# Kernel optimization log

Hardware: AMD Instinct MI355X
Metric: run time of the kernel (lower is better)

## Reference

```python
import jax, jax.numpy as jnp
import numpy as np

KERNEL_SIZE = 128
NEG_INF = -1e30


def setup_inputs() -> dict:
    key = jax.random.key(0)
    ks = jax.random.split(key, 5)
    B, S, D, H = 4, 4096, 512, 512
    x = jax.random.normal(ks[0], (B, S, D), dtype=jnp.float32)
    # torch nn.Linear weights: [out_features, in_features], y = x @ W.T + b
    Wq_w = jax.random.normal(ks[1], (H, D), dtype=jnp.float32) * (1.0 / np.sqrt(D))
    Wq_b = jax.random.normal(ks[2], (H,), dtype=jnp.float32) * 0.01
    Wk_w = jax.random.normal(ks[3], (H, D), dtype=jnp.float32) * (1.0 / np.sqrt(D))
    Wk_b = jax.random.normal(ks[4], (H,), dtype=jnp.float32) * 0.01
    return {"x": x, "Wq_w": Wq_w, "Wq_b": Wq_b, "Wk_w": Wk_w, "Wk_b": Wk_b}


def reference(x, Wq_w, Wq_b, Wk_w, Wk_b):
    # q, k: [B, S, H]
    q = jnp.einsum('bsd,hd->bsh', x, Wq_w) + Wq_b
    k = jnp.einsum('bsd,hd->bsh', x, Wk_w) + Wk_b
    # dense scores [B, S, S]
    scores = jnp.einsum('bih,bjh->bij', q, k)
    # band mask: True where i-kernel_size+1 <= j <= i+kernel_size-1
    idx = jnp.arange(x.shape[1])
    band = jnp.abs(idx[:, None] - idx[None, :]) < KERNEL_SIZE  # [S, S]
    scores = jnp.where(band[None, :, :], scores, NEG_INF)
    attn = jax.nn.softmax(scores, axis=2)
    # attend over raw x (no V projection in original module)
    return jnp.einsum('bij,bjd->bid', attn, x)
```

## Files before the change

kernel.cpp:

```cpp
#include <hip/hip_runtime.h>
#include <hip/hip_bf16.h>

#define S_LEN 4096
#define NEG_INF_F (-1e30f)

typedef __attribute__((ext_vector_type(4))) float f32x4;
typedef __attribute__((ext_vector_type(8))) short s16x8;
typedef unsigned short u16;

static __device__ __forceinline__ u16 f2bf(float f) {
    unsigned u = __builtin_bit_cast(unsigned, f);
    unsigned r = u + 0x7FFFu + ((u >> 16) & 1u);
    return (u16)(r >> 16);
}
static __device__ __forceinline__ float bf2f(u16 h) {
    unsigned u = ((unsigned)h) << 16;
    return __builtin_bit_cast(float, u);
}
static __device__ __forceinline__ void split4(const float4 v, ushort4& hi, ushort4& lo) {
    hi.x = f2bf(v.x); lo.x = f2bf(v.x - bf2f(hi.x));
    hi.y = f2bf(v.y); lo.y = f2bf(v.y - bf2f(hi.y));
    hi.z = f2bf(v.z); lo.z = f2bf(v.z - bf2f(hi.z));
    hi.w = f2bf(v.w); lo.w = f2bf(v.w - bf2f(hi.w));
}
static __device__ __forceinline__ void gl_lds16(const void* g, void* l) {
    __builtin_amdgcn_global_load_lds(
        (const __attribute__((address_space(1))) void*)g,
        (__attribute__((address_space(3))) void*)l, 16, 0, 0);
}
static __device__ __forceinline__ int swz64(int row, int col_u16) {
    return row * 64 + (col_u16 ^ ((row & 7) << 3));
}
static __device__ __forceinline__ int swz32(int row, int col_u16) {
    return row * 32 + (col_u16 ^ (((row >> 1) & 3) << 3));
}
static __device__ __forceinline__ int swz320(int row, int col_u16) {
    return row * 320 + (col_u16 ^ ((row & 7) << 3));
}
static __device__ __forceinline__ int xcd_swz512(int bid) {
    return (bid & 7) * 64 + (bid >> 3);
}
static __device__ __forceinline__ int xcd_swz256(int bid) {
    return (bid & 7) * 32 + (bid >> 3);
}

__global__ __launch_bounds__(256) void prep_kernel(
    const float* __restrict__ x, const float* __restrict__ Wk,
    const float* __restrict__ Wq, const float* __restrict__ bq,
    u16* __restrict__ xh, u16* __restrict__ xl, u16* __restrict__ xT,
    u16* __restrict__ Mth, u16* __restrict__ Mtl, float* __restrict__ uvec) {
    __shared__ __align__(16) u16 sm[9216];
    const int bid = blockIdx.x;
    const int tid = threadIdx.x;

    if (bid < 256) {
        const int bm = bid & 15, bn = bid >> 4;
        const int m0 = bm * 32, n0 = bn * 32;
        u16* Ath = sm;
        u16* Atl = sm + 2304;
        u16* Bth = sm + 4608;
        u16* Btl = sm + 6912;
        const int lane = tid & 63, w = tid >> 6;
        const int rg = w >> 1, cg = w & 1;
        const int frow = lane & 15, fk = (lane >> 4) * 8;
        f32x4 acc = {};

        for (int h0 = 0; h0 < 512; h0 += 64) {
            #pragma unroll
            for (int i = 0; i < 2; ++i) {
                int idx = i * 256 + tid;
                int h = idx >> 3, c4 = (idx & 7) * 4;
                float4 a = *(const float4*)(Wk + (size_t)(h0 + h) * 512 + m0 + c4);
                ushort4 ahi, alo; split4(a, ahi, alo);
                Ath[(c4 + 0) * 72 + h] = ahi.x; Atl[(c4 + 0) * 72 + h] = alo.x;
                Ath[(c4 + 1) * 72 + h] = ahi.y; Atl[(c4 + 1) * 72 + h] = alo.y;
                Ath[(c4 + 2) * 72 + h] = ahi.z; Atl[(c4 + 2) * 72 + h] = alo.z;
                Ath[(c4 + 3) * 72 + h] = ahi.w; Atl[(c4 + 3) * 72 + h] = alo.w;
                float4 b = *(const float4*)(Wq + (size_t)(h0 + h) * 512 + n0 + c4);
                ushort4 bhi, blo; split4(b, bhi, blo);
                Bth[(c4 + 0) * 72 + h] = bhi.x; Btl[(c4 + 0) * 72 + h] = blo.x;
                Bth[(c4 + 1) * 72 + h] = bhi.y; Btl[(c4 + 1) * 72 + h] = blo.y;
                Bth[(c4 + 2) * 72 + h] = bhi.z; Btl[(c4 + 2) * 72 + h] = blo.z;
                Bth[(c4 + 3) * 72 + h] = bhi.w; Btl[(c4 + 3) * 72 + h] = blo.w;
            }
            __syncthreads();
            #pragma unroll
            for (int kk = 0; kk < 2; ++kk) {
                s16x8 aH = *(const s16x8*)&Ath[(rg * 16 + frow) * 72 + kk * 32 + fk];
                s16x8 aL = *(const s16x8*)&Atl[(rg * 16 + frow) * 72 + kk * 32 + fk];
                s16x8 bH = *(const s16x8*)&Bth[(cg * 16 + frow) * 72 + kk * 32 + fk];
                s16x8 bL = *(const s16x8*)&Btl[(cg * 16 + frow) * 72 + kk * 32 + fk];
                acc = __builtin_amdgcn_mfma_f32_16x16x32_bf16(aH, bH, acc, 0, 0, 0);
                acc = __builtin_amdgcn_mfma_f32_16x16x32_bf16(aH, bL, acc, 0, 0, 0);
                acc = __builtin_amdgcn_mfma_f32_16x16x32_bf16(aL, bH, acc, 0, 0, 0);
            }
            __syncthreads();
        }
        int d1 = n0 + cg * 16 + frow;
        #pragma unroll
        for (int e = 0; e < 4; ++e) {
            int d2 = m0 + rg * 16 + (lane >> 4) * 4 + e;
            float v = acc[e];
            u16 hi = f2bf(v);
            Mth[(size_t)d2 * 512 + d1] = hi;
            Mtl[(size_t)d2 * 512 + d1] = f2bf(v - bf2f(hi));
        }
    } else if (bid < 264) {
        const int ub = bid - 256;
        float* red = (float*)sm;
        const int c = tid & 63, hg = tid >> 6;
        const int d2 = ub * 64 + c;
        float acc = 0.f;
        for (int h = hg; h < 512; h += 4) acc += Wk[(size_t)h * 512 + d2] * bq[h];
        red[hg * 64 + c] = acc;
        __syncthreads();
        if (hg == 0)
            uvec[d2] = red[0 * 64 + c] + red[1 * 64 + c] + red[2 * 64 + c] + red[3 * 64 + c];
    } else {
        const int sb = bid - 264;
        const int dt = sb & 7, st = (sb >> 3) & 63, b = sb >> 9;
        const int s0 = st * 64, d0 = dt * 64;
        u16 (*T)[74] = (u16(*)[74])sm;
        #pragma unroll
        for (int i = 0; i < 2; ++i) {
            int idx = i * 256 + tid;
            int r = idx >> 3, c8 = (idx & 7) * 8;
            const float* src = x + (size_t)(b * S_LEN + s0 + r) * 512 + d0 + c8;
            float4 v0 = *(const float4*)(src);
            float4 v1 = *(const float4*)(src + 4);
            ushort4 h0, l0, h1, l1;
            split4(v0, h0, l0);
            split4(v1, h1, l1);
            s16x8 hv, lv;
            hv[0] = (short)h0.x; hv[1] = (short)h0.y; hv[2] = (short)h0.z; hv[3] = (short)h0.w;
            hv[4] = (short)h1.x; hv[5] = (short)h1.y; hv[6] = (short)h1.z; hv[7] = (short)h1.w;
            lv[0] = (short)l0.x; lv[1] = (short)l0.y; lv[2] = (short)l0.z; lv[3] = (short)l0.w;
            lv[4] = (short)l1.x; lv[5] = (short)l1.y; lv[6] = (short)l1.z; lv[7] = (short)l1.w;
            *(s16x8*)(xh + (size_t)(b * S_LEN + s0 + r) * 512 + d0 + c8) = hv;
            *(s16x8*)(xl + (size_t)(b * S_LEN + s0 + r) * 512 + d0 + c8) = lv;
            unsigned* tp = (unsigned*)&T[r][c8];
            tp[0] = (unsigned)(u16)hv[0] | ((unsigned)(u16)hv[1] << 16);
            tp[1] = (unsigned)(u16)hv[2] | ((unsigned)(u16)hv[3] << 16);
            tp[2] = (unsigned)(u16)hv[4] | ((unsigned)(u16)hv[5] << 16);
            tp[3] = (unsigned)(u16)hv[6] | ((unsigned)(u16)hv[7] << 16);
        }
        __syncthreads();
        {
            const int drp = tid >> 3, sc = tid & 7;
            s16x8 v0, v1;
            #pragma unroll
            for (int t = 0; t < 8; ++t) {
                unsigned wv = *(const unsigned*)&T[sc * 8 + t][drp * 2];
                v0[t] = (short)(wv & 0xFFFFu);
                v1[t] = (short)(wv >> 16);
            }
            size_t base = (size_t)(b * 512 + d0 + drp * 2) * S_LEN + s0 + sc * 8;
            *(s16x8*)&xT[base] = v0;
            *(s16x8*)&xT[base + S_LEN] = v1;
        }
    }
}

__global__ __launch_bounds__(512) void z_kernel(
    const u16* __restrict__ xh, const u16* __restrict__ xl,
    const u16* __restrict__ Mth, const u16* __restrict__ Mtl,
    const float* __restrict__ u, u16* __restrict__ zh, u16* __restrict__ zl) {
    const int w_ = xcd_swz512((int)blockIdx.x);
    const int bm = w_ >> 2, bn = w_ & 3;
    const int m0 = bm * 128, n0 = bn * 128;
    __shared__ __align__(16) u16 Ah[128 * 64], Al[128 * 64];
    __shared__ __align__(16) u16 Bh[128 * 64], Bl[128 * 64];
    const int tid = threadIdx.x, lane = tid & 63, w = tid >> 6;
    const int rg = w >> 2, cg = w & 3;
    const int frow = lane & 15, fk = (lane >> 4) * 8;
    f32x4 acc[4][2] = {};

    for (int k0 = 0; k0 < 512; k0 += 64) {
        #pragma unroll
        for (int i = 0; i < 2; ++i) {
            int idx = i * 512 + tid;
            int r = idx >> 3, c = idx & 7;
            int sc = (c ^ (r & 7)) * 8;
            gl_lds16(xh + (size_t)(m0 + r) * 512 + k0 + sc, &Ah[idx * 8]);
            gl_lds16(xl + (size_t)(m0 + r) * 512 + k0 + sc, &Al[idx * 8]);
            gl_lds16(Mth + (size_t)(n0 + r) * 512 + k0 + sc, &Bh[idx * 8]);
            gl_lds16(Mtl + (size_t)(n0 + r) * 512 + k0 + sc, &Bl[idx * 8]);
        }
        __syncthreads();
        #pragma unroll
        for (int kk = 0; kk < 2; ++kk) {
            s16x8 aH[4], aL[4], bH[2], bL[2];
            #pragma unroll
            for (int mi = 0; mi < 4; ++mi) {
                int row = rg * 64 + mi * 16 + frow;
                aH[mi] = *(const s16x8*)&Ah[swz64(row, kk * 32 + fk)];
                aL[mi] = *(const s16x8*)&Al[swz64(row, kk * 32 + fk)];
            }
            #pragma unroll
            for (int ni = 0; ni < 2; ++ni) {
                int row = cg * 32 + ni * 16 + frow;
                bH[ni] = *(const s16x8*)&Bh[swz64(row, kk * 32 + fk)];
                bL[ni] = *(const s16x8*)&Bl[swz64(row, kk * 32 + fk)];
            }
            #pragma unroll
            for (int mi = 0; mi < 4; ++mi)
                #pragma unroll
                for (int ni = 0; ni < 2; ++ni) {
                    acc[mi][ni] = __builtin_amdgcn_mfma_f32_16x16x32_bf16(aH[mi], bH[ni], acc[mi][ni], 0, 0, 0);
                    acc[mi][ni] = __builtin_amdgcn_mfma_f32_16x16x32_bf16(aH[mi], bL[ni], acc[mi][ni], 0, 0, 0);
                    acc[mi][ni] = __builtin_amdgcn_mfma_f32_16x16x32_bf16(aL[mi], bH[ni], acc[mi][ni], 0, 0, 0);
                }
        }
        __syncthreads();
    }
    #pragma unroll
    for (int ni = 0; ni < 2; ++ni) {
        int col = n0 + cg * 32 + ni * 16 + frow;
        float uv = u[col];
        #pragma unroll
        for (int mi = 0; mi < 4; ++mi) {
            int rbase = m0 + rg * 64 + mi * 16 + (lane >> 4) * 4;
            #pragma unroll
            for (int e = 0; e < 4; ++e) {
                float v = acc[mi][ni][e] + uv;
                u16 hi = f2bf(v);
                zh[(size_t)(rbase + e) * 512 + col] = hi;
                zl[(size_t)(rbase + e) * 512 + col] = f2bf(v - bf2f(hi));
            }
        }
    }
}

__global__ __launch_bounds__(1024, 4) void attn_kernel(
    const u16* __restrict__ zh, const u16* __restrict__ zl,
    const u16* __restrict__ xh, const u16* __restrict__ xl,
    const u16* __restrict__ xT, float* __restrict__ out) {
    const int w_ = xcd_swz256((int)blockIdx.x);
    const int b = w_ >> 6, it = w_ & 63;
    const int i0 = it * 64, j0 = i0 - 128;
    const int mrow0 = b * S_LEN + i0;

    __shared__ __align__(16) u16 smem[61440];

    const int tid = threadIdx.x, lane = tid & 63, w = tid >> 6;
    const int g = w >> 2, q = w & 3;
    const int frow = lane & 15, fk = (lane >> 4) * 8;
    const int tstart = g + q * 4;
    const int nt = (q == 3) ? 5 : 4;
    const size_t qoff = (size_t)(mrow0 + g * 16 + frow) * 512;
    const int rq = (lane >> 4) * 4;

    f32x4 acc[5] = {};
    s16x8 kr[5];

    auto kload = [&](int s) {
        const int k0 = s * 64;
        #pragma unroll
        for (int i = 0; i < 5; ++i) {
            int f = i * 1024 + tid;
            int idx = (f < 2560) ? f : f - 2560;
            int r = idx >> 3, c = idx & 7;
            int j = min(max(j0 + r, 0), S_LEN - 1);
            const u16* src = (f < 2560) ? xh : xl;
            kr[i] = *(const s16x8*)(src + (size_t)(b * S_LEN + j) * 512 + k0 + c * 8);
        }
    };
    auto kwrite = [&]() {
        #pragma unroll
        for (int i = 0; i < 5; ++i) {
            int f = i * 1024 + tid;
            int idx = (f < 2560) ? f : f - 2560;
            int r = idx >> 3, c = idx & 7;
            int off = ((f < 2560) ? 0 : 20480) + swz64(r, c * 8);
            *(s16x8*)&smem[off] = kr[i];
        }
    };
    auto qkstep = [&](int t) {
        const int k0 = t * 64;
        s16x8 zH0 = *(const s16x8*)(zh + qoff + k0 + fk);
        s16x8 zH1 = *(const s16x8*)(zh + qoff + k0 + 32 + fk);
        s16x8 zL0 = *(const s16x8*)(zl + qoff + k0 + fk);
        s16x8 zL1 = *(const s16x8*)(zl + qoff + k0 + 32 + fk);
        __builtin_amdgcn_s_setprio(1);
        #pragma unroll
        for (int kk = 0; kk < 2; ++kk) {
            s16x8 aH = kk ? zH1 : zH0;
            s16x8 aL = kk ? zL1 : zL0;
            #pragma unroll
            for (int tt = 0; tt < 5; ++tt) {
                if (tt < nt) {
                    int krow = (tstart + tt) * 16 + frow;
                    s16x8 bH = *(const s16x8*)&smem[swz64(krow, kk * 32 + fk)];
                    s16x8 bL = *(const s16x8*)&smem[20480 + swz64(krow, kk * 32 + fk)];
                    acc[tt] = __builtin_amdgcn_mfma_f32_16x16x32_bf16(aH, bH, acc[tt], 0, 0, 0);
                    acc[tt] = __builtin_amdgcn_mfma_f32_16x16x32_bf16(aH, bL, acc[tt], 0, 0, 0);
                    acc[tt] = __builtin_amdgcn_mfma_f32_16x16x32_bf16(aL, bH, acc[tt], 0, 0, 0);
                }
            }
        }
        __builtin_amdgcn_s_setprio(0);
    };

    kload(0);
    for (int t = 0; t < 8; ++t) {
        __syncthreads();
        kwrite();
        __syncthreads();
        if (t < 7) kload(t + 1);
        qkstep(t);
    }

    s16x8 vreg[3];
    auto vload = [&](int ds) {
        const int d0 = ds * 64;
        #pragma unroll
        for (int i = 0; i < 3; ++i) {
            int f = i * 1024 + tid;
            if (f < 2560) {
                int dr = f / 40, c8 = f - dr * 40;
                int jb = j0 + c8 * 8;
                jb = min(max(jb, 0), S_LEN - 8);
                vreg[i] = *(const s16x8*)&xT[(size_t)(b * 512 + d0 + dr) * S_LEN + jb];
            }
        }
    };
    auto vwrite = [&](int vbase) {
        #pragma unroll
        for (int i = 0; i < 3; ++i) {
            int f = i * 1024 + tid;
            if (f < 2560) {
                int dr = f / 40, c8 = f - dr * 40;
                *(s16x8*)&smem[vbase + swz320(dr, c8 * 8)] = vreg[i];
            }
        }
    };
    vload(0);

    float* sred_max = (float*)&smem[40960];
    float* sred_sum = sred_max + 256;
    #pragma unroll
    for (int e = 0; e < 4; ++e) {
        int r = g * 16 + rq + e;
        float m = NEG_INF_F;
        #pragma unroll
        for (int tt = 0; tt < 5; ++tt) {
            if (tt < nt) {
                int jj = (tstart + tt) * 16 + frow;
                int dj = jj - r, j = j0 + jj;
                if (dj >= 1 && dj <= 255 && j >= 0 && j < S_LEN) m = fmaxf(m, acc[tt][e]);
            }
        }
        #pragma unroll
        for (int d = 1; d < 16; d <<= 1) m = fmaxf(m, __shfl_xor(m, d));
        if (frow == 0) sred_max[r * 4 + q] = m;
    }
    __syncthreads();
    float sh[4];
    #pragma unroll
    for (int e = 0; e < 4; ++e) {
        int r = g * 16 + rq + e;
        float mx = fmaxf(fmaxf(sred_max[r * 4], sred_max[r * 4 + 1]),
                         fmaxf(sred_max[r * 4 + 2], sred_max[r * 4 + 3]));
        float s = 0.f;
        #pragma unroll
        for (int tt = 0; tt < 5; ++tt) {
            float pv = 0.f;
            if (tt < nt) {
                int jj = (tstart + tt) * 16 + frow;
                int dj = jj - r, j = j0 + jj;
                bool valid = (dj >= 1 && dj <= 255 && j >= 0 && j < S_LEN);
                pv = valid ? __expf(acc[tt][e] - mx) : 0.f;
            }
            acc[tt][e] = pv;
            s += pv;
        }
        #pragma unroll
        for (int d = 1; d < 16; d <<= 1) s += __shfl_xor(s, d);
        sh[e] = s;
    }
    if (frow == 0) {
        #pragma unroll
        for (int e = 0; e < 4; ++e) sred_sum[(g * 16 + rq + e) * 4 + q] = sh[e];
    }
    __syncthreads();
    float invv[4];
    #pragma unroll
    for (int e = 0; e < 4; ++e) {
        int r = g * 16 + rq + e;
        invv[e] = 1.f / (sred_sum[r * 4] + sred_sum[r * 4 + 1] +
                         sred_sum[r * 4 + 2] + sred_sum[r * 4 + 3]);
    }
    __syncthreads();
    #pragma unroll
    for (int tt = 0; tt < 5; ++tt) {
        if (tt < nt) {
            int t = tstart + tt;
            #pragma unroll
            for (int e = 0; e < 4; ++e) {
                int r = g * 16 + rq + e;
                smem[swz320(r, t * 16 + frow)] = f2bf(acc[tt][e] * invv[e]);
            }
        }
    }
    if (q == 0) {
        for (int t = 0; t < g; ++t)
            #pragma unroll
            for (int e = 0; e < 4; ++e)
                smem[swz320(g * 16 + rq + e, t * 16 + frow)] = 0;
    }
    if (q == 3) {
        for (int t = g + 17; t < 20; ++t)
            #pragma unroll
            for (int e = 0; e < 4; ++e)
                smem[swz320(g * 16 + rq + e, t * 16 + frow)] = 0;
    }
    __syncthreads();

    vwrite(20480);
    vload(1);
    __syncthreads();

    s16x8 afrag[10];
    #pragma unroll
    for (int jt = 0; jt < 10; ++jt)
        afrag[jt] = *(const s16x8*)&smem[swz320(g * 16 + frow, jt * 32 + fk)];

    for (int ds = 0; ds < 8; ++ds) {
        const int cur = 20480 + (ds & 1) * 20480;
        const int nxt = 20480 + ((ds + 1) & 1) * 20480;
        if (ds < 7) {
            vwrite(nxt);
            if (ds < 6) vload(ds + 2);
        }
        f32x4 po = {};
        __builtin_amdgcn_s_setprio(1);
        #pragma unroll
        for (int jt = 0; jt < 10; ++jt) {
            s16x8 bv = *(const s16x8*)&smem[cur + swz320(q * 16 + frow, jt * 32 + fk)];
            po = __builtin_amdgcn_mfma_f32_16x16x32_bf16(afrag[jt], bv, po, 0, 0, 0);
        }
        __builtin_amdgcn_s_setprio(0);
        #pragma unroll
        for (int e = 0; e < 4; ++e) {
            int r = mrow0 + g * 16 + rq + e;
            out[(size_t)r * 512 + ds * 64 + q * 16 + frow] = po[e];
        }
        __syncthreads();
    }
}

extern "C" void kernel_launch(void* const* d_in, const int* in_sizes, int n_in,
                              void* d_out, int out_size, void* d_ws, size_t ws_size,
                              hipStream_t stream) {
    const float* x  = (const float*)d_in[0];
    const float* Wq = (const float*)d_in[1];
    const float* bq = (const float*)d_in[2];
    const float* Wk = (const float*)d_in[3];
    const float* bk = (const float*)d_in[4];
    (void)bk;
    float* out = (float*)d_out;

    u16* xh  = (u16*)d_ws;
    u16* xl  = xh + (size_t)8388608;
    u16* zh  = xl + (size_t)8388608;
    u16* zl  = zh + (size_t)8388608;
    u16* Mth = zl + (size_t)8388608;
    u16* Mtl = Mth + (size_t)262144;
    u16* xT  = Mtl + (size_t)262144;
    float* uv = (float*)(xT + (size_t)8388608);

    hipLaunchKernelGGL(prep_kernel, dim3(2312), dim3(256), 0, stream,
                       x, Wk, Wq, bq, xh, xl, xT, Mth, Mtl, uv);
    hipLaunchKernelGGL(z_kernel, dim3(512), dim3(512), 0, stream,
                       xh, xl, Mth, Mtl, uv, zh, zl);
    hipLaunchKernelGGL(attn_kernel, dim3(256), dim3(1024), 0, stream,
                       zh, zl, xh, xl, xT, out);
}
```

Baseline: 115.9 us.

## Move x transpose out of prep kernel into the z GEMM launch

The transposed bf16 copy of x (xT) is no longer built in the prep kernel. Extra blocks appended to the z GEMM kernel now build it, reading the bf16 xh already written by prep and transposing it through LDS, two tiles per 512-thread block. This shortens the prep kernel and lets the transpose fill the GEMM's grid, at the cost of re-reading xh from memory and a larger, mixed-role launch. The z GEMM blocks now use 64KB of shared memory held in one array.

```diff
diff --git a/kernel.cpp b/kernel.cpp
--- a/kernel.cpp
+++ b/kernel.cpp
@@ -31,9 +31,6 @@
 static __device__ __forceinline__ int swz64(int row, int col_u16) {
     return row * 64 + (col_u16 ^ ((row & 7) << 3));
 }
-static __device__ __forceinline__ int swz32(int row, int col_u16) {
-    return row * 32 + (col_u16 ^ (((row >> 1) & 3) << 3));
-}
 static __device__ __forceinline__ int swz320(int row, int col_u16) {
     return row * 320 + (col_u16 ^ ((row & 7) << 3));
 }
@@ -47,7 +44,7 @@
 __global__ __launch_bounds__(256) void prep_kernel(
     const float* __restrict__ x, const float* __restrict__ Wk,
     const float* __restrict__ Wq, const float* __restrict__ bq,
-    u16* __restrict__ xh, u16* __restrict__ xl, u16* __restrict__ xT,
+    u16* __restrict__ xh, u16* __restrict__ xl,
     u16* __restrict__ Mth, u16* __restrict__ Mtl, float* __restrict__ uvec) {
     __shared__ __align__(16) u16 sm[9216];
     const int bid = blockIdx.x;
@@ -120,7 +117,6 @@
         const int sb = bid - 264;
         const int dt = sb & 7, st = (sb >> 3) & 63, b = sb >> 9;
         const int s0 = st * 64, d0 = dt * 64;
-        u16 (*T)[74] = (u16(*)[74])sm;
         #pragma unroll
         for (int i = 0; i < 2; ++i) {
             int idx = i * 256 + tid;
@@ -138,15 +134,106 @@
             lv[4] = (short)l1.x; lv[5] = (short)l1.y; lv[6] = (short)l1.z; lv[7] = (short)l1.w;
             *(s16x8*)(xh + (size_t)(b * S_LEN + s0 + r) * 512 + d0 + c8) = hv;
             *(s16x8*)(xl + (size_t)(b * S_LEN + s0 + r) * 512 + d0 + c8) = lv;
+        }
+    }
+}
+
+__global__ __launch_bounds__(512) void zxt_kernel(
+    const u16* __restrict__ xh, const u16* __restrict__ xl,
+    const u16* __restrict__ Mth, const u16* __restrict__ Mtl,
+    const float* __restrict__ u, u16* __restrict__ zh, u16* __restrict__ zl,
+    u16* __restrict__ xT) {
+    __shared__ __align__(16) u16 sm[32768];
+    const int tid = threadIdx.x;
+
+    if (blockIdx.x < 512) {
+        const int w_ = xcd_swz512((int)blockIdx.x);
+        const int bm = w_ >> 2, bn = w_ & 3;
+        const int m0 = bm * 128, n0 = bn * 128;
+        u16* Ah = sm;
+        u16* Al = sm + 8192;
+        u16* Bh = sm + 16384;
+        u16* Bl = sm + 24576;
+        const int lane = tid & 63, w = tid >> 6;
+        const int rg = w >> 2, cg = w & 3;
+        const int frow = lane & 15, fk = (lane >> 4) * 8;
+        f32x4 acc[4][2] = {};
+
+        for (int k0 = 0; k0 < 512; k0 += 64) {
+            #pragma unroll
+            for (int i = 0; i < 2; ++i) {
+                int idx = i * 512 + tid;
+                int r = idx >> 3, c = idx & 7;
+                int sc = (c ^ (r & 7)) * 8;
+                gl_lds16(xh + (size_t)(m0 + r) * 512 + k0 + sc, &Ah[idx * 8]);
+                gl_lds16(xl + (size_t)(m0 + r) * 512 + k0 + sc, &Al[idx * 8]);
+                gl_lds16(Mth + (size_t)(n0 + r) * 512 + k0 + sc, &Bh[idx * 8]);
+                gl_lds16(Mtl + (size_t)(n0 + r) * 512 + k0 + sc, &Bl[idx * 8]);
+            }
+            __syncthreads();
+            #pragma unroll
+            for (int kk = 0; kk < 2; ++kk) {
+                s16x8 aH[4], aL[4], bH[2], bL[2];
+                #pragma unroll
+                for (int mi = 0; mi < 4; ++mi) {
+                    int row = rg * 64 + mi * 16 + frow;
+                    aH[mi] = *(const s16x8*)&Ah[swz64(row, kk * 32 + fk)];
+                    aL[mi] = *(const s16x8*)&Al[swz64(row, kk * 32 + fk)];
+                }
+                #pragma unroll
+                for (int ni = 0; ni < 2; ++ni) {
+                    int row = cg * 32 + ni * 16 + frow;
+                    bH[ni] = *(const s16x8*)&Bh[swz64(row, kk * 32 + fk)];
+                    bL[ni] = *(const s16x8*)&Bl[swz64(row, kk * 32 + fk)];
+                }
+                #pragma unroll
+                for (int mi = 0; mi < 4; ++mi)
+                    #pragma unroll
+                    for (int ni = 0; ni < 2; ++ni) {
+                        acc[mi][ni] = __builtin_amdgcn_mfma_f32_16x16x32_bf16(aH[mi], bH[ni], acc[mi][ni], 0, 0, 0);
+                        acc[mi][ni] = __builtin_amdgcn_mfma_f32_16x16x32_bf16(aH[mi], bL[ni], acc[mi][ni], 0, 0, 0);
+                        acc[mi][ni] = __builtin_amdgcn_mfma_f32_16x16x32_bf16(aL[mi], bH[ni], acc[mi][ni], 0, 0, 0);
+                    }
+            }
+            __syncthreads();
+        }
+        #pragma unroll
+        for (int ni = 0; ni < 2; ++ni) {
+            int col = n0 + cg * 32 + ni * 16 + frow;
+            float uv = u[col];
+            #pragma unroll
+            for (int mi = 0; mi < 4; ++mi) {
+                int rbase = m0 + rg * 64 + mi * 16 + (lane >> 4) * 4;
+                #pragma unroll
+                for (int e = 0; e < 4; ++e) {
+                    float v = acc[mi][ni][e] + uv;
+                    u16 hi = f2bf(v);
+                    zh[(size_t)(rbase + e) * 512 + col] = hi;
+                    zl[(size_t)(rbase + e) * 512 + col] = f2bf(v - bf2f(hi));
+                }
+            }
+        }
+    } else {
+        const int xb = (int)blockIdx.x - 512;
+        const int half = tid >> 8;
+        const int t256 = tid & 255;
+        const int tile = xb * 2 + half;
+        const int dt = tile & 7, st = (tile >> 3) & 63, b = tile >> 9;
+        const int s0 = st * 64, d0 = dt * 64;
+        u16 (*T)[74] = (u16(*)[74])(sm + half * 4736);
+
+        #pragma unroll
+        for (int i = 0; i < 2; ++i) {
+            int idx = i * 256 + t256;
+            int r = idx >> 3, c8 = (idx & 7) * 8;
+            s16x8 hv = *(const s16x8*)(xh + (size_t)(b * S_LEN + s0 + r) * 512 + d0 + c8);
+            const unsigned* hw = (const unsigned*)&hv;
             unsigned* tp = (unsigned*)&T[r][c8];
-            tp[0] = (unsigned)(u16)hv[0] | ((unsigned)(u16)hv[1] << 16);
-            tp[1] = (unsigned)(u16)hv[2] | ((unsigned)(u16)hv[3] << 16);
-            tp[2] = (unsigned)(u16)hv[4] | ((unsigned)(u16)hv[5] << 16);
-            tp[3] = (unsigned)(u16)hv[6] | ((unsigned)(u16)hv[7] << 16);
+            tp[0] = hw[0]; tp[1] = hw[1]; tp[2] = hw[2]; tp[3] = hw[3];
         }
         __syncthreads();
         {
-            const int drp = tid >> 3, sc = tid & 7;
+            const int drp = t256 >> 3, sc = t256 & 7;
             s16x8 v0, v1;
             #pragma unroll
             for (int t = 0; t < 8; ++t) {
@@ -157,76 +244,6 @@
             size_t base = (size_t)(b * 512 + d0 + drp * 2) * S_LEN + s0 + sc * 8;
             *(s16x8*)&xT[base] = v0;
             *(s16x8*)&xT[base + S_LEN] = v1;
-        }
-    }
-}
-
-__global__ __launch_bounds__(512) void z_kernel(
-    const u16* __restrict__ xh, const u16* __restrict__ xl,
-    const u16* __restrict__ Mth, const u16* __restrict__ Mtl,
-    const float* __restrict__ u, u16* __restrict__ zh, u16* __restrict__ zl) {
-    const int w_ = xcd_swz512((int)blockIdx.x);
-    const int bm = w_ >> 2, bn = w_ & 3;
-    const int m0 = bm * 128, n0 = bn * 128;
-    __shared__ __align__(16) u16 Ah[128 * 64], Al[128 * 64];
-    __shared__ __align__(16) u16 Bh[128 * 64], Bl[128 * 64];
-    const int tid = threadIdx.x, lane = tid & 63, w = tid >> 6;
-    const int rg = w >> 2, cg = w & 3;
-    const int frow = lane & 15, fk = (lane >> 4) * 8;
-    f32x4 acc[4][2] = {};
-
-    for (int k0 = 0; k0 < 512; k0 += 64) {
-        #pragma unroll
-        for (int i = 0; i < 2; ++i) {
-            int idx = i * 512 + tid;
-            int r = idx >> 3, c = idx & 7;
-            int sc = (c ^ (r & 7)) * 8;
-            gl_lds16(xh + (size_t)(m0 + r) * 512 + k0 + sc, &Ah[idx * 8]);
-            gl_lds16(xl + (size_t)(m0 + r) * 512 + k0 + sc, &Al[idx * 8]);
-            gl_lds16(Mth + (size_t)(n0 + r) * 512 + k0 + sc, &Bh[idx * 8]);
-            gl_lds16(Mtl + (size_t)(n0 + r) * 512 + k0 + sc, &Bl[idx * 8]);
-        }
-        __syncthreads();
-        #pragma unroll
-        for (int kk = 0; kk < 2; ++kk) {
-            s16x8 aH[4], aL[4], bH[2], bL[2];
-            #pragma unroll
-            for (int mi = 0; mi < 4; ++mi) {
-                int row = rg * 64 + mi * 16 + frow;
-                aH[mi] = *(const s16x8*)&Ah[swz64(row, kk * 32 + fk)];
-                aL[mi] = *(const s16x8*)&Al[swz64(row, kk * 32 + fk)];
-            }
-            #pragma unroll
-            for (int ni = 0; ni < 2; ++ni) {
-                int row = cg * 32 + ni * 16 + frow;
-                bH[ni] = *(const s16x8*)&Bh[swz64(row, kk * 32 + fk)];
-                bL[ni] = *(const s16x8*)&Bl[swz64(row, kk * 32 + fk)];
-            }
-            #pragma unroll
-            for (int mi = 0; mi < 4; ++mi)
-                #pragma unroll
-                for (int ni = 0; ni < 2; ++ni) {
-                    acc[mi][ni] = __builtin_amdgcn_mfma_f32_16x16x32_bf16(aH[mi], bH[ni], acc[mi][ni], 0, 0, 0);
-                    acc[mi][ni] = __builtin_amdgcn_mfma_f32_16x16x32_bf16(aH[mi], bL[ni], acc[mi][ni], 0, 0, 0);
-                    acc[mi][ni] = __builtin_amdgcn_mfma_f32_16x16x32_bf16(aL[mi], bH[ni], acc[mi][ni], 0, 0, 0);
-                }
-        }
-        __syncthreads();
-    }
-    #pragma unroll
-    for (int ni = 0; ni < 2; ++ni) {
-        int col = n0 + cg * 32 + ni * 16 + frow;
-        float uv = u[col];
-        #pragma unroll
-        for (int mi = 0; mi < 4; ++mi) {
-            int rbase = m0 + rg * 64 + mi * 16 + (lane >> 4) * 4;
-            #pragma unroll
-            for (int e = 0; e < 4; ++e) {
-                float v = acc[mi][ni][e] + uv;
-                u16 hi = f2bf(v);
-                zh[(size_t)(rbase + e) * 512 + col] = hi;
-                zl[(size_t)(rbase + e) * 512 + col] = f2bf(v - bf2f(hi));
-            }
         }
     }
 }
@@ -470,9 +487,9 @@
     float* uv = (float*)(xT + (size_t)8388608);
 
     hipLaunchKernelGGL(prep_kernel, dim3(2312), dim3(256), 0, stream,
-                       x, Wk, Wq, bq, xh, xl, xT, Mth, Mtl, uv);
-    hipLaunchKernelGGL(z_kernel, dim3(512), dim3(512), 0, stream,
-                       xh, xl, Mth, Mtl, uv, zh, zl);
+                       x, Wk, Wq, bq, xh, xl, Mth, Mtl, uv);
+    hipLaunchKernelGGL(zxt_kernel, dim3(1536), dim3(512), 0, stream,
+                       xh, xl, Mth, Mtl, uv, zh, zl, xT);
     hipLaunchKernelGGL(attn_kernel, dim3(256), dim3(1024), 0, stream,
                        zh, zl, xh, xl, xT, out);
 }
```

After: 119.0 us. +2.6%, slower.
